# Kernel tuning notes

Hardware: AMD Instinct MI355X
Metric: run time of the kernel (lower is better)

The kernel has to match this reference:

```python
import jax, jax.numpy as jnp
import numpy as np


def setup_inputs() -> dict:
    key = jax.random.key(0)
    ks = jax.random.split(key, 8)
    b, l, d_model = 2, 2048, 1024
    d_inner, d_state, dt_rank, d_conv = 2048, 16, 64, 4
    g = lambda k, shape, s: jax.random.normal(k, shape, jnp.float32) * s
    A = jnp.broadcast_to(jnp.arange(1, d_state + 1, dtype=jnp.float32), (d_inner, d_state))
    return {
        "x": g(ks[0], (b, l, d_model), 1.0),
        "W_in": g(ks[1], (d_model, 2 * d_inner), 0.02),
        "W_conv": g(ks[2], (d_inner, 1, d_conv), 0.1),
        "b_conv": g(ks[3], (d_inner,), 0.1),
        "W_x": g(ks[4], (d_inner, dt_rank + 2 * d_state), 0.02),
        "W_dt": g(ks[5], (dt_rank, d_inner), 0.02),
        "b_dt": g(ks[6], (d_inner,), 0.1),
        "A_log": jnp.log(A),
        "D": jnp.ones((d_inner,), jnp.float32),
        "W_out": g(ks[7], (d_inner, d_model), 0.02),
    }


def _selective_scan(x, delta, A, B, C, D):
    # x, delta: (b, l, d); A: (d, n); B, C: (b, l, n); D: (d,)
    b, l, d = x.shape
    n = A.shape[1]

    def step(h, inp):
        dt, Bt, Ct, xt = inp  # (b,d), (b,n), (b,n), (b,d)
        dA = jnp.exp(dt[:, :, None] * A)                     # (b,d,n)
        h = dA * h + (dt * xt)[:, :, None] * Bt[:, None, :]  # (b,d,n)
        y = jnp.einsum('bdn,bn->bd', h, Ct)
        return h, y

    h0 = jnp.zeros((b, d, n), x.dtype)
    xs = (jnp.swapaxes(delta, 0, 1), jnp.swapaxes(B, 0, 1),
          jnp.swapaxes(C, 0, 1), jnp.swapaxes(x, 0, 1))
    _, ys = jax.lax.scan(step, h0, xs)   # ys: (l, b, d)
    return jnp.swapaxes(ys, 0, 1) + D * x


def _mamba(x, W_in, W_conv, b_conv, W_x, W_dt, b_dt, A_log, D, W_out):
    b, l, _ = x.shape
    d_inner = W_conv.shape[0]
    d_conv = W_conv.shape[2]
    dt_rank = W_dt.shape[0]
    n = A_log.shape[1]

    xr = x @ W_in                                   # (b,l,2*d_inner)
    xin, res = xr[..., :d_inner], xr[..., d_inner:]

    # depthwise causal conv1d (left pad d_conv-1 == torch pad both + trim to l)
    xc = jnp.swapaxes(xin, 1, 2)                    # (b,d_inner,l)
    xc = jax.lax.conv_general_dilated(
        xc, W_conv, window_strides=(1,), padding=[(d_conv - 1, 0)],
        feature_group_count=d_inner,
        dimension_numbers=('NCH', 'OIH', 'NCH')) + b_conv[None, :, None]
    xs = jax.nn.silu(jnp.swapaxes(xc, 1, 2))        # (b,l,d_inner)

    x_dbl = xs @ W_x                                # (b,l,dt_rank+2n)
    delta = jax.nn.softplus(x_dbl[..., :dt_rank] @ W_dt + b_dt)
    Bm = x_dbl[..., dt_rank:dt_rank + n]
    Cm = x_dbl[..., dt_rank + n:]
    A = -jnp.exp(A_log)

    y = _selective_scan(xs, delta, A, Bm, Cm, D)
    y = y * jax.nn.silu(res)
    return y @ W_out


def reference(x, W_in, W_conv, b_conv, W_x, W_dt, b_dt, A_log, D, W_out):
    return _mamba(x, W_in, W_conv, b_conv, W_x, W_dt, b_dt, A_log, D, W_out)
```

## Files before the change

kernel.cpp:

```cpp
#include <hip/hip_runtime.h>


typedef unsigned short ushort_t;
using short8 = __attribute__((ext_vector_type(8))) short;
using f32x4  = __attribute__((ext_vector_type(4))) float;
using gptr_t = const __attribute__((address_space(1))) unsigned short*;
using sptr_t = __attribute__((address_space(3))) unsigned short*;

#define NC 64
#define CL 32

__device__ inline ushort_t f2bf(float v) {
    unsigned u = __float_as_uint(v);
    unsigned r = (u + 0x7fff + ((u >> 16) & 1)) >> 16;
    return (ushort_t)r;
}
__device__ inline float bf2f(ushort_t h) { return __uint_as_float(((unsigned)h) << 16); }
__device__ inline void split2(float v, ushort_t& h, ushort_t& l) {
    h = f2bf(v);
    l = f2bf(v - bf2f(h));
}


__global__ void split_plain4(const float* __restrict__ in, ushort_t* __restrict__ h,
                             ushort_t* __restrict__ l, int n4) {
    int i = blockIdx.x * blockDim.x + threadIdx.x;
    if (i >= n4) return;
    float4 v = ((const float4*)in)[i];
    ushort4 hh, ll;
    split2(v.x, hh.x, ll.x); split2(v.y, hh.y, ll.y);
    split2(v.z, hh.z, ll.z); split2(v.w, hh.w, ll.w);
    ((ushort4*)h)[i] = hh;
    ((ushort4*)l)[i] = ll;
}

__global__ __launch_bounds__(256) void split_transpose(
    const float* __restrict__ W, ushort_t* __restrict__ Th, ushort_t* __restrict__ Tl,
    int K, int N) {
    __shared__ float tile[32][33];
    int n0 = blockIdx.x * 32, k0 = blockIdx.y * 32;
    int tx = threadIdx.x & 31, ty = threadIdx.x >> 5;
    #pragma unroll
    for (int j = 0; j < 4; ++j) {
        int k = ty + j * 8;
        tile[k][tx] = (n0 + tx < N) ? W[(size_t)(k0 + k) * N + n0 + tx] : 0.f;
    }
    __syncthreads();
    #pragma unroll
    for (int j = 0; j < 4; ++j) {
        int nrow = ty + j * 8;
        float v = tile[tx][nrow];
        ushort_t h, l;
        split2(v, h, l);
        size_t o = (size_t)(n0 + nrow) * K + k0 + tx;
        Th[o] = h; Tl[o] = l;
    }
}

__global__ __launch_bounds__(256) void gemm_mfma3(
    const ushort_t* __restrict__ Ah, const ushort_t* __restrict__ Al,
    const ushort_t* __restrict__ Bh, const ushort_t* __restrict__ Bl,
    float* __restrict__ C, int M, int N, int K,
    const float* __restrict__ bias, int epi) {
    __shared__ ushort_t sAh[4096], sAl[4096], sBh[4096], sBl[4096];
    const int tid  = threadIdx.x;
    const int wid  = tid >> 6;
    const int lane = tid & 63;
    int bx = blockIdx.x, by = blockIdx.y;
    {
        int nwg = gridDim.x * gridDim.y;
        if ((nwg & 7) == 0) {
            int flat = by * gridDim.x + bx;
            int swz = (flat & 7) * (nwg >> 3) + (flat >> 3);
            bx = swz % gridDim.x;
            by = swz / gridDim.x;
        }
    }
    const int bm = by * 128;
    const int bn = bx * 128;
    const int wr = wid >> 1, wc = wid & 1;

    f32x4 acc[4][4];
    #pragma unroll
    for (int i = 0; i < 4; ++i)
        #pragma unroll
        for (int j = 0; j < 4; ++j) acc[i][j] = (f32x4){0.f, 0.f, 0.f, 0.f};

    for (int k0 = 0; k0 < K; k0 += 32) {
        #pragma unroll
        for (int issue = 0; issue < 2; ++issue) {
            const int off = wid * 2048 + issue * 1024 + lane * 16;
            const int row = off >> 6;
            const int ce  = (off & 63) >> 1;
            const size_t ga = (size_t)(bm + row) * K + k0 + ce;
            const size_t gb = (size_t)(bn + row) * K + k0 + ce;
            const int lo = (wid * 2048 + issue * 1024) >> 1;
            __builtin_amdgcn_global_load_lds((gptr_t)(Ah + ga), (sptr_t)&sAh[lo], 16, 0, 0);
            __builtin_amdgcn_global_load_lds((gptr_t)(Al + ga), (sptr_t)&sAl[lo], 16, 0, 0);
            __builtin_amdgcn_global_load_lds((gptr_t)(Bh + gb), (sptr_t)&sBh[lo], 16, 0, 0);
            __builtin_amdgcn_global_load_lds((gptr_t)(Bl + gb), (sptr_t)&sBl[lo], 16, 0, 0);
        }
        __syncthreads();

        const int fr = lane & 15;
        const int kb = (lane >> 4) * 8;
        short8 ah[4], al[4], bh[4], bl[4];
        #pragma unroll
        for (int i = 0; i < 4; ++i) {
            const int ra = (wr * 64 + i * 16 + fr) * 32 + kb;
            ah[i] = *(const short8*)&sAh[ra];
            al[i] = *(const short8*)&sAl[ra];
            const int rb = (wc * 64 + i * 16 + fr) * 32 + kb;
            bh[i] = *(const short8*)&sBh[rb];
            bl[i] = *(const short8*)&sBl[rb];
        }
        #pragma unroll
        for (int i = 0; i < 4; ++i)
            #pragma unroll
            for (int j = 0; j < 4; ++j) {
                acc[i][j] = __builtin_amdgcn_mfma_f32_16x16x32_bf16(ah[i], bh[j], acc[i][j], 0, 0, 0);
                acc[i][j] = __builtin_amdgcn_mfma_f32_16x16x32_bf16(ah[i], bl[j], acc[i][j], 0, 0, 0);
                acc[i][j] = __builtin_amdgcn_mfma_f32_16x16x32_bf16(al[i], bh[j], acc[i][j], 0, 0, 0);
            }
        __syncthreads();
    }

    #pragma unroll
    for (int i = 0; i < 4; ++i) {
        int row = bm + wr * 64 + i * 16 + (lane >> 4) * 4;
        #pragma unroll
        for (int j = 0; j < 4; ++j) {
            int col = bn + wc * 64 + j * 16 + (lane & 15);
            float* cp = C + (size_t)row * N + col;
            #pragma unroll
            for (int r = 0; r < 4; ++r) {
                float v = acc[i][j][r];
                if (epi == 1) {
                    v += bias[col];
                    v = (v > 20.f) ? v : log1pf(__expf(v));
                }
                cp[(size_t)r * N] = v;
            }
        }
    }
}

__global__ __launch_bounds__(256) void gemm_mfma3_n64(
    const ushort_t* __restrict__ Ah, const ushort_t* __restrict__ Al,
    const ushort_t* __restrict__ Bh, const ushort_t* __restrict__ Bl,
    float* __restrict__ C, int M, int N, int K) {
    __shared__ ushort_t sAh[4096], sAl[4096], sBh[2048], sBl[2048];
    const int tid  = threadIdx.x;
    const int wid  = tid >> 6;
    const int lane = tid & 63;
    int bx = blockIdx.x, by = blockIdx.y;
    {
        int nwg = gridDim.x * gridDim.y;
        if ((nwg & 7) == 0) {
            int flat = by * gridDim.x + bx;
            int swz = (flat & 7) * (nwg >> 3) + (flat >> 3);
            bx = swz % gridDim.x;
            by = swz / gridDim.x;
        }
    }
    const int bm = by * 128;
    const int bn = bx * 64;
    const int wr = wid >> 1, wc = wid & 1;

    f32x4 acc[4][2];
    #pragma unroll
    for (int i = 0; i < 4; ++i)
        #pragma unroll
        for (int j = 0; j < 2; ++j) acc[i][j] = (f32x4){0.f, 0.f, 0.f, 0.f};

    for (int k0 = 0; k0 < K; k0 += 32) {
        #pragma unroll
        for (int issue = 0; issue < 2; ++issue) {
            const int off = issue * 4096 + tid * 16;
            const int row = off >> 6;
            const int ce  = (off & 63) >> 1;
            const size_t ga = (size_t)(bm + row) * K + k0 + ce;
            const int lo = (issue * 4096 + wid * 1024) >> 1;
            __builtin_amdgcn_global_load_lds((gptr_t)(Ah + ga), (sptr_t)&sAh[lo], 16, 0, 0);
            __builtin_amdgcn_global_load_lds((gptr_t)(Al + ga), (sptr_t)&sAl[lo], 16, 0, 0);
        }
        {
            const int off = tid * 16;
            const int row = off >> 6;
            const int ce  = (off & 63) >> 1;
            const size_t gb = (size_t)(bn + row) * K + k0 + ce;
            const int lo = (wid * 1024) >> 1;
            __builtin_amdgcn_global_load_lds((gptr_t)(Bh + gb), (sptr_t)&sBh[lo], 16, 0, 0);
            __builtin_amdgcn_global_load_lds((gptr_t)(Bl + gb), (sptr_t)&sBl[lo], 16, 0, 0);
        }
        __syncthreads();

        const int fr = lane & 15;
        const int kb = (lane >> 4) * 8;
        short8 ah[4], al[4], bh[2], bl[2];
        #pragma unroll
        for (int i = 0; i < 4; ++i) {
            const int ra = (wr * 64 + i * 16 + fr) * 32 + kb;
            ah[i] = *(const short8*)&sAh[ra];
            al[i] = *(const short8*)&sAl[ra];
        }
        #pragma unroll
        for (int j = 0; j < 2; ++j) {
            const int rb = (wc * 32 + j * 16 + fr) * 32 + kb;
            bh[j] = *(const short8*)&sBh[rb];
            bl[j] = *(const short8*)&sBl[rb];
        }
        #pragma unroll
        for (int i = 0; i < 4; ++i)
            #pragma unroll
            for (int j = 0; j < 2; ++j) {
                acc[i][j] = __builtin_amdgcn_mfma_f32_16x16x32_bf16(ah[i], bh[j], acc[i][j], 0, 0, 0);
                acc[i][j] = __builtin_amdgcn_mfma_f32_16x16x32_bf16(ah[i], bl[j], acc[i][j], 0, 0, 0);
                acc[i][j] = __builtin_amdgcn_mfma_f32_16x16x32_bf16(al[i], bh[j], acc[i][j], 0, 0, 0);
            }
        __syncthreads();
    }

    #pragma unroll
    for (int i = 0; i < 4; ++i) {
        int row = bm + wr * 64 + i * 16 + (lane >> 4) * 4;
        #pragma unroll
        for (int j = 0; j < 2; ++j) {
            int col = bn + wc * 32 + j * 16 + (lane & 15);
            float* cp = C + (size_t)row * N + col;
            #pragma unroll
            for (int r = 0; r < 4; ++r) cp[(size_t)r * N] = acc[i][j][r];
        }
    }
}

__global__ __launch_bounds__(256) void gemm_mfma3_sk(
    const ushort_t* __restrict__ Ah, const ushort_t* __restrict__ Al,
    const ushort_t* __restrict__ Bh, const ushort_t* __restrict__ Bl,
    float* __restrict__ partial, int K) {
    __shared__ ushort_t sAh[4096], sAl[4096], sBh[4096], sBl[4096];
    const int tid  = threadIdx.x;
    const int wid  = tid >> 6;
    const int lane = tid & 63;
    const int kslice = blockIdx.x;
    const int bm = blockIdx.y * 128;
    const int wr = wid >> 1, wc = wid & 1;
    const int kbeg = kslice * 256;

    f32x4 acc[4][4];
    #pragma unroll
    for (int i = 0; i < 4; ++i)
        #pragma unroll
        for (int j = 0; j < 4; ++j) acc[i][j] = (f32x4){0.f, 0.f, 0.f, 0.f};

    for (int k0 = kbeg; k0 < kbeg + 256; k0 += 32) {
        #pragma unroll
        for (int issue = 0; issue < 2; ++issue) {
            const int off = wid * 2048 + issue * 1024 + lane * 16;
            const int row = off >> 6;
            const int ce  = (off & 63) >> 1;
            const size_t ga = (size_t)(bm + row) * K + k0 + ce;
            const size_t gb = (size_t)row * K + k0 + ce;
            const int lo = (wid * 2048 + issue * 1024) >> 1;
            __builtin_amdgcn_global_load_lds((gptr_t)(Ah + ga), (sptr_t)&sAh[lo], 16, 0, 0);
            __builtin_amdgcn_global_load_lds((gptr_t)(Al + ga), (sptr_t)&sAl[lo], 16, 0, 0);
            __builtin_amdgcn_global_load_lds((gptr_t)(Bh + gb), (sptr_t)&sBh[lo], 16, 0, 0);
            __builtin_amdgcn_global_load_lds((gptr_t)(Bl + gb), (sptr_t)&sBl[lo], 16, 0, 0);
        }
        __syncthreads();

        const int fr = lane & 15;
        const int kb = (lane >> 4) * 8;
        short8 ah[4], al[4], bh[4], bl[4];
        #pragma unroll
        for (int i = 0; i < 4; ++i) {
            const int ra = (wr * 64 + i * 16 + fr) * 32 + kb;
            ah[i] = *(const short8*)&sAh[ra];
            al[i] = *(const short8*)&sAl[ra];
            const int rb = (wc * 64 + i * 16 + fr) * 32 + kb;
            bh[i] = *(const short8*)&sBh[rb];
            bl[i] = *(const short8*)&sBl[rb];
        }
        #pragma unroll
        for (int i = 0; i < 4; ++i)
            #pragma unroll
            for (int j = 0; j < 4; ++j) {
                acc[i][j] = __builtin_amdgcn_mfma_f32_16x16x32_bf16(ah[i], bh[j], acc[i][j], 0, 0, 0);
                acc[i][j] = __builtin_amdgcn_mfma_f32_16x16x32_bf16(ah[i], bl[j], acc[i][j], 0, 0, 0);
                acc[i][j] = __builtin_amdgcn_mfma_f32_16x16x32_bf16(al[i], bh[j], acc[i][j], 0, 0, 0);
            }
        __syncthreads();
    }

    float* Cp = partial + (size_t)kslice * 4096 * 128;
    #pragma unroll
    for (int i = 0; i < 4; ++i) {
        int row = bm + wr * 64 + i * 16 + (lane >> 4) * 4;
        #pragma unroll
        for (int j = 0; j < 4; ++j) {
            int col = wc * 64 + j * 16 + (lane & 15);
            float* cp = Cp + (size_t)row * 128 + col;
            #pragma unroll
            for (int r = 0; r < 4; ++r) cp[(size_t)r * 128] = acc[i][j][r];
        }
    }
}

__global__ void reduce8split(const float4* __restrict__ p, float4* __restrict__ outp,
                             ushort_t* __restrict__ dh, ushort_t* __restrict__ dl) {
    int i = blockIdx.x * 256 + threadIdx.x;
    float4 s = p[i];
    #pragma unroll
    for (int k = 1; k < 8; ++k) {
        float4 v = p[i + k * 131072];
        s.x += v.x; s.y += v.y; s.z += v.z; s.w += v.w;
    }
    outp[i] = s;
    int c4 = i & 31;
    if (c4 < 16) {
        int row = i >> 5;
        ushort4 hh, ll;
        split2(s.x, hh.x, ll.x); split2(s.y, hh.y, ll.y);
        split2(s.z, hh.z, ll.z); split2(s.w, hh.w, ll.w);
        ((ushort4*)dh)[row * 16 + c4] = hh;
        ((ushort4*)dl)[row * 16 + c4] = ll;
    }
}

__global__ void conv_silu_k(const float* __restrict__ xr, const float* __restrict__ Wc,
                            const float* __restrict__ bc,
                            ushort_t* __restrict__ xsh, ushort_t* __restrict__ xsl,
                            int total) {
    for (int idx = blockIdx.x * blockDim.x + threadIdx.x; idx < total;
         idx += gridDim.x * blockDim.x) {
        int d = idx & 2047;
        int l = (idx >> 11) & 2047;
        int b = idx >> 22;
        float acc = bc[d];
        const float* wp = Wc + d * 4;
        #pragma unroll
        for (int k = 0; k < 4; ++k) {
            int ll = l - 3 + k;
            if (ll >= 0)
                acc = fmaf(xr[((size_t)(b * 2048 + ll) << 12) + d], wp[k], acc);
        }
        float v = acc / (1.f + __expf(-acc));
        ushort_t h, lo;
        split2(v, h, lo);
        xsh[idx] = h;
        xsl[idx] = lo;
    }
}


__global__ __launch_bounds__(256) void scan_p1(
    const float* __restrict__ delta,
    const ushort_t* __restrict__ xsh, const ushort_t* __restrict__ xsl,
    const float* __restrict__ xdbl, const float* __restrict__ A_log,
    float* __restrict__ S, float* __restrict__ sumdt) {
    const int u = blockIdx.x * 256 + threadIdx.x;
    const int chunk = u >> 12;
    const int c = u & 4095;
    const int b = c >> 11, d = c & 2047;

    float a[16];
    #pragma unroll
    for (int i = 0; i < 4; ++i) {
        float4 v = ((const float4*)(A_log + d * 16))[i];
        a[4 * i + 0] = -__expf(v.x); a[4 * i + 1] = -__expf(v.y);
        a[4 * i + 2] = -__expf(v.z); a[4 * i + 3] = -__expf(v.w);
    }
    float h[16];
    #pragma unroll
    for (int n = 0; n < 16; ++n) h[n] = 0.f;
    float sdt = 0.f;

    const size_t row0 = (size_t)b * 2048 + (size_t)chunk * CL;
    const float4* xd4 = (const float4*)xdbl;
    #pragma unroll 2
    for (int t = 0; t < CL; ++t) {
        const size_t row = row0 + t;
        float dt = delta[row * 2048 + d];
        float xv = bf2f(xsh[row * 2048 + d]) + bf2f(xsl[row * 2048 + d]);
        float4 Bv[4];
        #pragma unroll
        for (int i = 0; i < 4; ++i) Bv[i] = xd4[row * 32 + 16 + i];
        const float* Bf = (const float*)Bv;
        sdt += dt;
        float du = dt * xv;
        #pragma unroll
        for (int n = 0; n < 16; ++n) {
            float dA = __expf(dt * a[n]);
            h[n] = fmaf(dA, h[n], du * Bf[n]);
        }
    }
    float4* S4 = (float4*)(S + ((size_t)chunk * 4096 + c) * 16);
    #pragma unroll
    for (int i = 0; i < 4; ++i)
        S4[i] = make_float4(h[4 * i + 0], h[4 * i + 1], h[4 * i + 2], h[4 * i + 3]);
    sumdt[chunk * 4096 + c] = sdt;
}

__global__ __launch_bounds__(256) void scan_p2(
    float* __restrict__ S, const float* __restrict__ sumdt,
    const float* __restrict__ A_log) {
    const int idx = blockIdx.x * blockDim.x + threadIdx.x;
    const int n = idx & 15;
    const int c = (idx >> 4) & 4095;
    const int d = c & 2047;
    const float a = -__expf(A_log[d * 16 + n]);
    float h = 0.f;
    for (int k = 0; k < NC; ++k) {
        const size_t o = ((size_t)k * 4096 + c) * 16 + n;
        float carry = S[o];
        S[o] = h;
        float P = __expf(a * sumdt[k * 4096 + c]);
        h = fmaf(P, h, carry);
    }
}

__global__ __launch_bounds__(256) void scan_p3(
    const float* __restrict__ delta,
    const ushort_t* __restrict__ xsh, const ushort_t* __restrict__ xsl,
    const float* __restrict__ xdbl, const float* __restrict__ xr,
    const float* __restrict__ A_log, const float* __restrict__ Dp,
    const float* __restrict__ H0,
    ushort_t* __restrict__ yh, ushort_t* __restrict__ yl) {
    const int u = blockIdx.x * 256 + threadIdx.x;
    const int chunk = u >> 12;
    const int c = u & 4095;
    const int b = c >> 11, d = c & 2047;

    float a[16];
    #pragma unroll
    for (int i = 0; i < 4; ++i) {
        float4 v = ((const float4*)(A_log + d * 16))[i];
        a[4 * i + 0] = -__expf(v.x); a[4 * i + 1] = -__expf(v.y);
        a[4 * i + 2] = -__expf(v.z); a[4 * i + 3] = -__expf(v.w);
    }
    float h[16];
    const float4* H4 = (const float4*)(H0 + ((size_t)chunk * 4096 + c) * 16);
    #pragma unroll
    for (int i = 0; i < 4; ++i) {
        float4 v = H4[i];
        h[4 * i + 0] = v.x; h[4 * i + 1] = v.y; h[4 * i + 2] = v.z; h[4 * i + 3] = v.w;
    }
    const float Dd = Dp[d];

    const size_t row0 = (size_t)b * 2048 + (size_t)chunk * CL;
    const float4* xd4 = (const float4*)xdbl;
    #pragma unroll 2
    for (int t = 0; t < CL; ++t) {
        const size_t row = row0 + t;
        float dt = delta[row * 2048 + d];
        float xv = bf2f(xsh[row * 2048 + d]) + bf2f(xsl[row * 2048 + d]);
        float4 BC[8];
        #pragma unroll
        for (int i = 0; i < 8; ++i) BC[i] = xd4[row * 32 + 16 + i];
        const float* Bf = (const float*)BC;
        const float* Cf = Bf + 16;
        float du = dt * xv;
        float acc = 0.f;
        #pragma unroll
        for (int n = 0; n < 16; ++n) {
            float dA = __expf(dt * a[n]);
            h[n] = fmaf(dA, h[n], du * Bf[n]);
            acc = fmaf(h[n], Cf[n], acc);
        }
        float rv = xr[(row << 12) + 2048 + d];
        float yv = fmaf(Dd, xv, acc) * (rv / (1.f + __expf(-rv)));
        ushort_t hb, lb;
        split2(yv, hb, lb);
        yh[row * 2048 + d] = hb;
        yl[row * 2048 + d] = lb;
    }
}

extern "C" void kernel_launch(void* const* d_in, const int* in_sizes, int n_in,
                              void* d_out, int out_size, void* d_ws, size_t ws_size,
                              hipStream_t stream) {
    const float* x      = (const float*)d_in[0];
    const float* W_in   = (const float*)d_in[1];
    const float* W_conv = (const float*)d_in[2];
    const float* b_conv = (const float*)d_in[3];
    const float* W_x    = (const float*)d_in[4];
    const float* W_dt   = (const float*)d_in[5];
    const float* b_dt   = (const float*)d_in[6];
    const float* A_log  = (const float*)d_in[7];
    const float* Dp     = (const float*)d_in[8];
    const float* W_out  = (const float*)d_in[9];
    float* out = (float*)d_out;

    float* ws    = (float*)d_ws;
    float* xr    = ws;
    float* xdbl  = xr + 16777216;
    float* delta = xdbl + 524288;
    float* S     = delta + 8388608;
    float* sumdt = S + 4194304;
    ushort_t* base = (ushort_t*)(sumdt + 262144);
    ushort_t* xh = base, *xl = base + 4194304;
    ushort_t* winh = base + 8388608, *winl = base + 12582912;
    float*    partial = (float*)base;
    ushort_t* yh = base, *yl = base + 8388608;
    ushort_t* wouth = base + 16777216, *woutl = base + 18874368;
    ushort_t* wxh   = base + 20971520, *wxl   = base + 21233664;
    ushort_t* wdth  = base + 21495808, *wdtl  = base + 21626880;
    ushort_t* dAh   = base + 21757952, *dAl   = base + 22020096;
    ushort_t* xsh   = base + 22282240, *xsl   = base + 30670848;

    dim3 blk(256);

    split_plain4<<<dim3(4096), blk, 0, stream>>>(x, xh, xl, 1048576);
    split_transpose<<<dim3(128, 32), blk, 0, stream>>>(W_in, winh, winl, 1024, 4096);
    split_transpose<<<dim3(32, 64), blk, 0, stream>>>(W_out, wouth, woutl, 2048, 1024);
    split_transpose<<<dim3(4, 64), blk, 0, stream>>>(W_x, wxh, wxl, 2048, 96);
    split_transpose<<<dim3(64, 2), blk, 0, stream>>>(W_dt, wdth, wdtl, 64, 2048);

    gemm_mfma3<<<dim3(32, 32), blk, 0, stream>>>(xh, xl, winh, winl, xr,
                                                 4096, 4096, 1024, nullptr, 0);
    conv_silu_k<<<dim3(4096), blk, 0, stream>>>(xr, W_conv, b_conv, xsh, xsl, 8388608);
    gemm_mfma3_sk<<<dim3(8, 32), blk, 0, stream>>>(xsh, xsl, wxh, wxl, partial, 2048);
    reduce8split<<<dim3(512), blk, 0, stream>>>((const float4*)partial, (float4*)xdbl,
                                                dAh, dAl);
    gemm_mfma3<<<dim3(16, 32), blk, 0, stream>>>(dAh, dAl, wdth, wdtl, delta,
                                                 4096, 2048, 64, b_dt, 1);
    scan_p1<<<dim3(1024), blk, 0, stream>>>(delta, xsh, xsl, xdbl, A_log, S, sumdt);
    scan_p2<<<dim3(256), blk, 0, stream>>>(S, sumdt, A_log);
    scan_p3<<<dim3(1024), blk, 0, stream>>>(delta, xsh, xsl, xdbl, xr, A_log, Dp, S, yh, yl);
    gemm_mfma3_n64<<<dim3(16, 32), blk, 0, stream>>>(yh, yl, wouth, woutl, out,
                                                     4096, 1024, 2048);
}
```

Before: 541.0 us.

## Merge weight conversions into one launch, drop tile swizzle, deepen split-K

Replaces five separate split/transpose launches with one kernel that dispatches on block index, cutting launch overhead. Removes the grouped workgroup swizzle from the two main GEMMs and uses plain row-major block order. Doubles the split-K factor of the W_x GEMM to 16 slices of 128, stores only the 96 real columns of each partial, and reduces them with a 16-way reduce kernel. The risks are L2 locality lost from the swizzle and the extra partial traffic from more slices.

New measurement: 525.5 us. 1.03x faster.

```diff
diff --git a/kernel.cpp b/kernel.cpp
--- a/kernel.cpp
+++ b/kernel.cpp
@@ -21,24 +21,34 @@
     l = f2bf(v - bf2f(h));
 }
 
-
-__global__ void split_plain4(const float* __restrict__ in, ushort_t* __restrict__ h,
-                             ushort_t* __restrict__ l, int n4) {
-    int i = blockIdx.x * blockDim.x + threadIdx.x;
-    if (i >= n4) return;
-    float4 v = ((const float4*)in)[i];
-    ushort4 hh, ll;
-    split2(v.x, hh.x, ll.x); split2(v.y, hh.y, ll.y);
-    split2(v.z, hh.z, ll.z); split2(v.w, hh.w, ll.w);
-    ((ushort4*)h)[i] = hh;
-    ((ushort4*)l)[i] = ll;
-}
-
-__global__ __launch_bounds__(256) void split_transpose(
-    const float* __restrict__ W, ushort_t* __restrict__ Th, ushort_t* __restrict__ Tl,
-    int K, int N) {
+__global__ __launch_bounds__(256) void convert_all(
+    const float* __restrict__ x, ushort_t* __restrict__ xh, ushort_t* __restrict__ xl,
+    const float* __restrict__ W_in, ushort_t* __restrict__ winh, ushort_t* __restrict__ winl,
+    const float* __restrict__ W_out, ushort_t* __restrict__ wouth, ushort_t* __restrict__ woutl,
+    const float* __restrict__ W_x, ushort_t* __restrict__ wxh, ushort_t* __restrict__ wxl,
+    const float* __restrict__ W_dt, ushort_t* __restrict__ wdth, ushort_t* __restrict__ wdtl) {
     __shared__ float tile[32][33];
-    int n0 = blockIdx.x * 32, k0 = blockIdx.y * 32;
+    const int id = blockIdx.x;
+    if (id < 4096) {
+        int i = id * 256 + threadIdx.x;
+        float4 v = ((const float4*)x)[i];
+        ushort4 hh, ll;
+        split2(v.x, hh.x, ll.x); split2(v.y, hh.y, ll.y);
+        split2(v.z, hh.z, ll.z); split2(v.w, hh.w, ll.w);
+        ((ushort4*)xh)[i] = hh;
+        ((ushort4*)xl)[i] = ll;
+        return;
+    }
+    const float* W; ushort_t *Th, *Tl; int K, N, bx, by;
+    if (id < 8192)       { W = W_in;  Th = winh;  Tl = winl;  K = 1024; N = 4096;
+                           bx = (id - 4096) & 127; by = (id - 4096) >> 7; }
+    else if (id < 10240) { W = W_out; Th = wouth; Tl = woutl; K = 2048; N = 1024;
+                           bx = (id - 8192) & 31;  by = (id - 8192) >> 5; }
+    else if (id < 10496) { W = W_x;   Th = wxh;   Tl = wxl;   K = 2048; N = 96;
+                           bx = (id - 10240) & 3;  by = (id - 10240) >> 2; }
+    else                 { W = W_dt;  Th = wdth;  Tl = wdtl;  K = 64;   N = 2048;
+                           bx = (id - 10496) & 63; by = (id - 10496) >> 6; }
+    int n0 = bx * 32, k0 = by * 32;
     int tx = threadIdx.x & 31, ty = threadIdx.x >> 5;
     #pragma unroll
     for (int j = 0; j < 4; ++j) {
@@ -66,18 +76,8 @@
     const int tid  = threadIdx.x;
     const int wid  = tid >> 6;
     const int lane = tid & 63;
-    int bx = blockIdx.x, by = blockIdx.y;
-    {
-        int nwg = gridDim.x * gridDim.y;
-        if ((nwg & 7) == 0) {
-            int flat = by * gridDim.x + bx;
-            int swz = (flat & 7) * (nwg >> 3) + (flat >> 3);
-            bx = swz % gridDim.x;
-            by = swz / gridDim.x;
-        }
-    }
-    const int bm = by * 128;
-    const int bn = bx * 128;
+    const int bm = blockIdx.y * 128;
+    const int bn = blockIdx.x * 128;
     const int wr = wid >> 1, wc = wid & 1;
 
     f32x4 acc[4][4];
@@ -153,18 +153,8 @@
     const int tid  = threadIdx.x;
     const int wid  = tid >> 6;
     const int lane = tid & 63;
-    int bx = blockIdx.x, by = blockIdx.y;
-    {
-        int nwg = gridDim.x * gridDim.y;
-        if ((nwg & 7) == 0) {
-            int flat = by * gridDim.x + bx;
-            int swz = (flat & 7) * (nwg >> 3) + (flat >> 3);
-            bx = swz % gridDim.x;
-            by = swz / gridDim.x;
-        }
-    }
-    const int bm = by * 128;
-    const int bn = bx * 64;
+    const int bm = blockIdx.y * 128;
+    const int bn = blockIdx.x * 64;
     const int wr = wid >> 1, wc = wid & 1;
 
     f32x4 acc[4][2];
@@ -245,7 +235,7 @@
     const int kslice = blockIdx.x;
     const int bm = blockIdx.y * 128;
     const int wr = wid >> 1, wc = wid & 1;
-    const int kbeg = kslice * 256;
+    const int kbeg = kslice * 128;
 
     f32x4 acc[4][4];
     #pragma unroll
@@ -253,7 +243,7 @@
         #pragma unroll
         for (int j = 0; j < 4; ++j) acc[i][j] = (f32x4){0.f, 0.f, 0.f, 0.f};
 
-    for (int k0 = kbeg; k0 < kbeg + 256; k0 += 32) {
+    for (int k0 = kbeg; k0 < kbeg + 128; k0 += 32) {
         #pragma unroll
         for (int issue = 0; issue < 2; ++issue) {
             const int off = wid * 2048 + issue * 1024 + lane * 16;
@@ -292,33 +282,35 @@
         __syncthreads();
     }
 
-    float* Cp = partial + (size_t)kslice * 4096 * 128;
+    float* Cp = partial + (size_t)kslice * 4096 * 96;
     #pragma unroll
     for (int i = 0; i < 4; ++i) {
         int row = bm + wr * 64 + i * 16 + (lane >> 4) * 4;
         #pragma unroll
         for (int j = 0; j < 4; ++j) {
             int col = wc * 64 + j * 16 + (lane & 15);
-            float* cp = Cp + (size_t)row * 128 + col;
-            #pragma unroll
-            for (int r = 0; r < 4; ++r) cp[(size_t)r * 128] = acc[i][j][r];
-        }
-    }
-}
-
-__global__ void reduce8split(const float4* __restrict__ p, float4* __restrict__ outp,
-                             ushort_t* __restrict__ dh, ushort_t* __restrict__ dl) {
+            if (col < 96) {
+                float* cp = Cp + (size_t)row * 96 + col;
+                #pragma unroll
+                for (int r = 0; r < 4; ++r) cp[(size_t)r * 96] = acc[i][j][r];
+            }
+        }
+    }
+}
+
+__global__ void reduce16split(const float4* __restrict__ p, float4* __restrict__ xdbl4,
+                              ushort_t* __restrict__ dh, ushort_t* __restrict__ dl) {
     int i = blockIdx.x * 256 + threadIdx.x;
     float4 s = p[i];
     #pragma unroll
-    for (int k = 1; k < 8; ++k) {
-        float4 v = p[i + k * 131072];
+    for (int k = 1; k < 16; ++k) {
+        float4 v = p[i + k * 98304];
         s.x += v.x; s.y += v.y; s.z += v.z; s.w += v.w;
     }
-    outp[i] = s;
-    int c4 = i & 31;
+    int row = i / 24;
+    int c4  = i - row * 24;
+    xdbl4[row * 32 + c4] = s;
     if (c4 < 16) {
-        int row = i >> 5;
         ushort4 hh, ll;
         split2(s.x, hh.x, ll.x); split2(s.y, hh.y, ll.y);
         split2(s.z, hh.z, ll.z); split2(s.w, hh.w, ll.w);
@@ -510,18 +502,16 @@
 
     dim3 blk(256);
 
-    split_plain4<<<dim3(4096), blk, 0, stream>>>(x, xh, xl, 1048576);
-    split_transpose<<<dim3(128, 32), blk, 0, stream>>>(W_in, winh, winl, 1024, 4096);
-    split_transpose<<<dim3(32, 64), blk, 0, stream>>>(W_out, wouth, woutl, 2048, 1024);
-    split_transpose<<<dim3(4, 64), blk, 0, stream>>>(W_x, wxh, wxl, 2048, 96);
-    split_transpose<<<dim3(64, 2), blk, 0, stream>>>(W_dt, wdth, wdtl, 64, 2048);
+    convert_all<<<dim3(10624), blk, 0, stream>>>(x, xh, xl, W_in, winh, winl,
+                                                 W_out, wouth, woutl,
+                                                 W_x, wxh, wxl, W_dt, wdth, wdtl);
 
     gemm_mfma3<<<dim3(32, 32), blk, 0, stream>>>(xh, xl, winh, winl, xr,
                                                  4096, 4096, 1024, nullptr, 0);
     conv_silu_k<<<dim3(4096), blk, 0, stream>>>(xr, W_conv, b_conv, xsh, xsl, 8388608);
-    gemm_mfma3_sk<<<dim3(8, 32), blk, 0, stream>>>(xsh, xsl, wxh, wxl, partial, 2048);
-    reduce8split<<<dim3(512), blk, 0, stream>>>((const float4*)partial, (float4*)xdbl,
-                                                dAh, dAl);
+    gemm_mfma3_sk<<<dim3(16, 32), blk, 0, stream>>>(xsh, xsl, wxh, wxl, partial, 2048);
+    reduce16split<<<dim3(384), blk, 0, stream>>>((const float4*)partial, (float4*)xdbl,
+                                                 dAh, dAl);
     gemm_mfma3<<<dim3(16, 32), blk, 0, stream>>>(dAh, dAl, wdth, wdtl, delta,
                                                  4096, 2048, 64, b_dt, 1);
     scan_p1<<<dim3(1024), blk, 0, stream>>>(delta, xsh, xsl, xdbl, A_log, S, sumdt);
```
